# Performance work log

Hardware: AMD Instinct MI355X
Metric: run time of the kernel (lower is better)

## Reference

```python
import jax, jax.numpy as jnp
import numpy as np

TEMPERATURE = 2.0


def _safe_l2(diff):
    # l2 norm over last axis, safe at zero (diagonal) so it matches norm(2,-1) forward
    s = jnp.sum(diff * diff, axis=-1)
    return jnp.sqrt(jnp.where(s > 0, s, 1.0)) * (s > 0)


def _offdiag_cols(n):
    # column indices of off-diagonal elements per row, matching
    # masked_select((1-eye).bool()).view(n, n-1) row-major ordering
    k = jnp.arange(n - 1)[None, :]          # [1, n-1]
    i = jnp.arange(n)[:, None]              # [n, 1]
    return k + (k >= i)                     # [n, n-1]


def setup_inputs() -> dict:
    key = jax.random.key(0)
    kf, kl = jax.random.split(key)
    features = jax.random.normal(kf, (512, 128), dtype=jnp.float32)
    labels = jax.random.normal(kl, (256, 2), dtype=jnp.float32)
    return {"features": features, "labels": labels}


def reference(features, labels):
    labels2 = jnp.concatenate([labels, labels], axis=0)  # labels.repeat(2,1)
    # label diff: l1 pairwise  [n, n]
    label_diffs = jnp.abs(labels2[:, None, :] - labels2[None, :, :]).sum(-1)
    # feature sim: negative l2 pairwise, divided by temperature  [n, n]
    logits = -_safe_l2(features[:, None, :] - features[None, :, :]) / TEMPERATURE
    n = logits.shape[0]

    rows = jnp.arange(n)[:, None]
    cols = _offdiag_cols(n)
    logits_od = logits[rows, cols]            # [n, n-1]
    ld_od = label_diffs[rows, cols]           # [n, n-1]

    logits_max = jax.lax.stop_gradient(jnp.max(logits_od, axis=1, keepdims=True))
    logits_od = logits_od - logits_max
    exp_logits = jnp.exp(logits_od)           # [n, n-1]

    # neg_mask[i, k, j] = label_diffs[i, j] >= label_diffs[i, k]
    neg_mask = ld_od[:, None, :] >= ld_od[:, :, None]          # [n, n-1, n-1] bool
    denom = jnp.einsum('ikj,ij->ik', neg_mask.astype(exp_logits.dtype), exp_logits)
    log_probs = logits_od - jnp.log(denom)    # [n, n-1]
    loss = -jnp.sum(log_probs) / (n * (n - 1))
    return loss
```

## Files before the change

kernel.cpp:

```cpp
#include <hip/hip_runtime.h>
#include <math.h>

#define N 512
#define C 256
#define D 128

__global__ __launch_bounds__(256) void k1_logits(const float* __restrict__ feat,
                                                 const float* __restrict__ labels,
                                                 float* __restrict__ lg,
                                                 float* __restrict__ ld2) {
    const int tid = threadIdx.x;

    {
        const int i0 = blockIdx.x << 1;
#pragma unroll
        for (int e = tid; e < 2 * C; e += 256) {
            const int row = i0 + (e >> 8);
            const int cc  = e & 255;
            const float2 lc2 = ((const float2*)labels)[cc];
            const float2 li2 = ((const float2*)labels)[row & 255];
            ld2[(size_t)row * C + cc] = fabsf(li2.x - lc2.x) + fabsf(li2.y - lc2.y);
        }
    }

    const int row0 = (blockIdx.x >> 4) << 5;
    const int col0 = (blockIdx.x & 15) << 5;

    __shared__ float4 As[32][32];
    __shared__ float4 Bs[32][32];

    const float4* f4 = (const float4*)feat;
    {
        const int r = tid >> 5, c4 = tid & 31;
#pragma unroll
        for (int p = 0; p < 4; ++p) {
            const int rr = r + p * 8;
            const int sc = c4 ^ ((rr >> 1) & 7);
            As[rr][sc] = f4[(size_t)(row0 + rr) * 32 + c4];
            Bs[rr][sc] = f4[(size_t)(col0 + rr) * 32 + c4];
        }
    }
    __syncthreads();

    const int ty = tid >> 4, tx = tid & 15;
    const int r0 = 2 * ty, r1 = 2 * ty + 1;
    const int c0 = 2 * tx, c1 = 2 * tx + 1;
    const int sa = ty & 7, sb = tx & 7;

    float s00 = 0.f, s01 = 0.f, s10 = 0.f, s11 = 0.f;
#pragma unroll 8
    for (int q = 0; q < 32; ++q) {
        float4 a0 = As[r0][q ^ sa];
        float4 a1 = As[r1][q ^ sa];
        float4 b0 = Bs[c0][q ^ sb];
        float4 b1 = Bs[c1][q ^ sb];
        float t;
        t = a0.x - b0.x; s00 = fmaf(t, t, s00);
        t = a0.y - b0.y; s00 = fmaf(t, t, s00);
        t = a0.z - b0.z; s00 = fmaf(t, t, s00);
        t = a0.w - b0.w; s00 = fmaf(t, t, s00);
        t = a0.x - b1.x; s01 = fmaf(t, t, s01);
        t = a0.y - b1.y; s01 = fmaf(t, t, s01);
        t = a0.z - b1.z; s01 = fmaf(t, t, s01);
        t = a0.w - b1.w; s01 = fmaf(t, t, s01);
        t = a1.x - b0.x; s10 = fmaf(t, t, s10);
        t = a1.y - b0.y; s10 = fmaf(t, t, s10);
        t = a1.z - b0.z; s10 = fmaf(t, t, s10);
        t = a1.w - b0.w; s10 = fmaf(t, t, s10);
        t = a1.x - b1.x; s11 = fmaf(t, t, s11);
        t = a1.y - b1.y; s11 = fmaf(t, t, s11);
        t = a1.z - b1.z; s11 = fmaf(t, t, s11);
        t = a1.w - b1.w; s11 = fmaf(t, t, s11);
    }
    float l00 = (s00 > 0.f) ? -0.5f * sqrtf(s00) : 0.f;
    float l01 = (s01 > 0.f) ? -0.5f * sqrtf(s01) : 0.f;
    float l10 = (s10 > 0.f) ? -0.5f * sqrtf(s10) : 0.f;
    float l11 = (s11 > 0.f) ? -0.5f * sqrtf(s11) : 0.f;

    *(float2*)(lg + (size_t)(row0 + r0) * N + col0 + c0) = make_float2(l00, l01);
    *(float2*)(lg + (size_t)(row0 + r1) * N + col0 + c0) = make_float2(l10, l11);
}

__global__ __launch_bounds__(256) void k23_row(const float* __restrict__ lg,
                                               const float* __restrict__ ld2,
                                               float* __restrict__ rowout) {
    const int i = blockIdx.x;
    const int c = threadIdx.x;

    __shared__ alignas(16) float sev[C];
    __shared__ float redm[4], reds[4], redl[4];
    __shared__ float lci;

    const float la = lg[(size_t)i * N + c];
    const float lb = lg[(size_t)i * N + c + 256];

    float m = -1e30f;
    if (c != i) m = la;
    if (c + 256 != i) m = fmaxf(m, lb);
#pragma unroll
    for (int off = 32; off > 0; off >>= 1) m = fmaxf(m, __shfl_xor(m, off, 64));
    if ((c & 63) == 0) redm[c >> 6] = m;
    __syncthreads();
    m = fmaxf(fmaxf(redm[0], redm[1]), fmaxf(redm[2], redm[3]));

    const float ea = (c == i) ? 0.f : __expf(la - m);
    const float eb = (c + 256 == i) ? 0.f : __expf(lb - m);
    sev[c] = ea + eb;

    float s = la + lb;
#pragma unroll
    for (int off = 32; off > 0; off >>= 1) s += __shfl_xor(s, off, 64);
    if ((c & 63) == 0) reds[c >> 6] = s;
    __syncthreads();
    const float rowsum = (reds[0] + reds[1] + reds[2] + reds[3]) - 511.f * m;

    const float* __restrict__ rl = ld2 + (size_t)i * C;
    const float ldk = rl[c];
    const float4* e4 = (const float4*)sev;
    float d0 = 0.f, d1 = 0.f, d2 = 0.f, d3 = 0.f;
#pragma unroll 8
    for (int q = 0; q < C / 4; ++q) {
        const float a0 = rl[4 * q + 0], a1 = rl[4 * q + 1];
        const float a2 = rl[4 * q + 2], a3 = rl[4 * q + 3];
        const float4 ev = e4[q];
        d0 += (a0 >= ldk) ? ev.x : 0.f;
        d1 += (a1 >= ldk) ? ev.y : 0.f;
        d2 += (a2 >= ldk) ? ev.z : 0.f;
        d3 += (a3 >= ldk) ? ev.w : 0.f;
    }
    const float lden = __logf((d0 + d1) + (d2 + d3));

    if (c == (i & 255)) lci = lden;
    float t = lden;
#pragma unroll
    for (int off = 32; off > 0; off >>= 1) t += __shfl_xor(t, off, 64);
    if ((c & 63) == 0) redl[c >> 6] = t;
    __syncthreads();
    if (c == 0) {
        const float tot = redl[0] + redl[1] + redl[2] + redl[3];
        rowout[i] = rowsum - (2.f * tot - lci);
    }
}

__global__ __launch_bounds__(256) void k4_reduce(const float* __restrict__ rowout,
                                                 float* __restrict__ out) {
    const int tid = threadIdx.x;
    double s = 0.0;
    for (int j = tid; j < N; j += 256) s += (double)rowout[j];
#pragma unroll
    for (int off = 32; off > 0; off >>= 1) s += __shfl_down(s, off, 64);
    __shared__ double sd[4];
    if ((tid & 63) == 0) sd[tid >> 6] = s;
    __syncthreads();
    if (tid == 0) {
        double t = sd[0] + sd[1] + sd[2] + sd[3];
        out[0] = (float)(-t / ((double)N * (double)(N - 1)));
    }
}

extern "C" void kernel_launch(void* const* d_in, const int* in_sizes, int n_in,
                              void* d_out, int out_size, void* d_ws, size_t ws_size,
                              hipStream_t stream) {
    const float* feat   = (const float*)d_in[0];
    const float* labels = (const float*)d_in[1];
    float* out = (float*)d_out;

    float* lg     = (float*)d_ws;
    float* ld2    = lg + (size_t)N * N;
    float* rowout = ld2 + (size_t)N * C;

    k1_logits<<<256, 256, 0, stream>>>(feat, labels, lg, ld2);
    k23_row <<<N,   256, 0, stream>>>(lg, ld2, rowout);
    k4_reduce<<<1,  256, 0, stream>>>(rowout, out);
}
```

Baseline: 18.90 us.

## Replace O(C^2) masked denominator sum with rank-sorted prefix scan

k1 now computes, for each label row, a per-column rank (count of strictly smaller label distances plus a tie-broken full rank) instead of storing raw label distances. k23 scatters the exp values into shared memory in descending rank order and runs a Hillis-Steele prefix scan, then reads the denominator at the min-rank position, replacing the 256-iteration masked accumulation per thread. This trades the quadratic work in the row kernel for 8 scan steps with barriers, while k1 takes on the quadratic rank count once per label row. Exact float ties rely on the min-rank lookup to keep the >= semantics, and the summation order differs from before.

```diff
diff --git a/kernel.cpp b/kernel.cpp
--- a/kernel.cpp
+++ b/kernel.cpp
@@ -8,23 +8,33 @@
 __global__ __launch_bounds__(256) void k1_logits(const float* __restrict__ feat,
                                                  const float* __restrict__ labels,
                                                  float* __restrict__ lg,
-                                                 float* __restrict__ ld2) {
+                                                 int* __restrict__ ranks) {
     const int tid = threadIdx.x;
+    const int b = blockIdx.x;
 
+    __shared__ alignas(16) float sld[C];
     {
-        const int i0 = blockIdx.x << 1;
-#pragma unroll
-        for (int e = tid; e < 2 * C; e += 256) {
-            const int row = i0 + (e >> 8);
-            const int cc  = e & 255;
-            const float2 lc2 = ((const float2*)labels)[cc];
-            const float2 li2 = ((const float2*)labels)[row & 255];
-            ld2[(size_t)row * C + cc] = fabsf(li2.x - lc2.x) + fabsf(li2.y - lc2.y);
+        const float2 lr = ((const float2*)labels)[b];
+        const float2 lc = ((const float2*)labels)[tid];
+        const float ldc = fabsf(lr.x - lc.x) + fabsf(lr.y - lc.y);
+        sld[tid] = ldc;
+        __syncthreads();
+        int clt = 0, ceq = 0;
+        const float4* s4 = (const float4*)sld;
+#pragma unroll 8
+        for (int q = 0; q < C / 4; ++q) {
+            const float4 a = s4[q];
+            const int j0 = 4 * q;
+            clt += (a.x < ldc); ceq += (a.x == ldc && (j0 + 0) < tid);
+            clt += (a.y < ldc); ceq += (a.y == ldc && (j0 + 1) < tid);
+            clt += (a.z < ldc); ceq += (a.z == ldc && (j0 + 2) < tid);
+            clt += (a.w < ldc); ceq += (a.w == ldc && (j0 + 3) < tid);
         }
+        ranks[b * C + tid] = (clt << 16) | (clt + ceq);
     }
 
-    const int row0 = (blockIdx.x >> 4) << 5;
-    const int col0 = (blockIdx.x & 15) << 5;
+    const int row0 = (b >> 4) << 5;
+    const int col0 = (b & 15) << 5;
 
     __shared__ float4 As[32][32];
     __shared__ float4 Bs[32][32];
@@ -82,12 +92,13 @@
 }
 
 __global__ __launch_bounds__(256) void k23_row(const float* __restrict__ lg,
-                                               const float* __restrict__ ld2,
+                                               const int* __restrict__ ranks,
                                                float* __restrict__ rowout) {
     const int i = blockIdx.x;
     const int c = threadIdx.x;
 
-    __shared__ alignas(16) float sev[C];
+    __shared__ alignas(16) float sa_[C];
+    __shared__ alignas(16) float sb_[C];
     __shared__ float redm[4], reds[4], redl[4];
     __shared__ float lci;
 
@@ -105,7 +116,13 @@
 
     const float ea = (c == i) ? 0.f : __expf(la - m);
     const float eb = (c + 256 == i) ? 0.f : __expf(lb - m);
-    sev[c] = ea + eb;
+    const float sev = ea + eb;
+
+    const int pk = ranks[(size_t)(i & 255) * C + c];
+    const int minrank  = pk >> 16;
+    const int fullrank = pk & 0xffff;
+
+    sa_[255 - fullrank] = sev;
 
     float s = la + lb;
 #pragma unroll
@@ -114,21 +131,18 @@
     __syncthreads();
     const float rowsum = (reds[0] + reds[1] + reds[2] + reds[3]) - 511.f * m;
 
-    const float* __restrict__ rl = ld2 + (size_t)i * C;
-    const float ldk = rl[c];
-    const float4* e4 = (const float4*)sev;
-    float d0 = 0.f, d1 = 0.f, d2 = 0.f, d3 = 0.f;
-#pragma unroll 8
-    for (int q = 0; q < C / 4; ++q) {
-        const float a0 = rl[4 * q + 0], a1 = rl[4 * q + 1];
-        const float a2 = rl[4 * q + 2], a3 = rl[4 * q + 3];
-        const float4 ev = e4[q];
-        d0 += (a0 >= ldk) ? ev.x : 0.f;
-        d1 += (a1 >= ldk) ? ev.y : 0.f;
-        d2 += (a2 >= ldk) ? ev.z : 0.f;
-        d3 += (a3 >= ldk) ? ev.w : 0.f;
+    float* src = sa_;
+    float* dst = sb_;
+#pragma unroll
+    for (int off = 1; off < C; off <<= 1) {
+        float v = src[c];
+        if (c >= off) v += src[c - off];
+        dst[c] = v;
+        __syncthreads();
+        float* tmp = src; src = dst; dst = tmp;
     }
-    const float lden = __logf((d0 + d1) + (d2 + d3));
+    const float den  = src[255 - minrank];
+    const float lden = __logf(den);
 
     if (c == (i & 255)) lci = lden;
     float t = lden;
@@ -166,10 +180,10 @@
     float* out = (float*)d_out;
 
     float* lg     = (float*)d_ws;
-    float* ld2    = lg + (size_t)N * N;
-    float* rowout = ld2 + (size_t)N * C;
+    int*   ranks  = (int*)(lg + (size_t)N * N);
+    float* rowout = (float*)(ranks + 256 * C);
 
-    k1_logits<<<256, 256, 0, stream>>>(feat, labels, lg, ld2);
-    k23_row <<<N,   256, 0, stream>>>(lg, ld2, rowout);
+    k1_logits<<<256, 256, 0, stream>>>(feat, labels, lg, ranks);
+    k23_row <<<N,   256, 0, stream>>>(lg, ranks, rowout);
     k4_reduce<<<1,  256, 0, stream>>>(rowout, out);
 }
```

Result: slower. 22.30 us (+18.0%).
